# Kernel tuning notes

Measured on AMD Instinct MI355X. Metric: run time of the kernel, lower is better.

The kernel has to match this reference:

```python
import jax, jax.numpy as jnp
import numpy as np

DELTA = 1.5
EPS = 1e-7  # torch-em dice_score denominator clamp


def shift2d(t, off):
    # Equivalent to torch-em ReplicationPad + slice on the (already inverted)
    # offset: shifted[..., i, j] = t[..., clip(i + oy, 0, H-1), clip(j + ox, 0, W-1)]
    H, W = t.shape[-2], t.shape[-1]
    iy = jnp.clip(jnp.arange(H) + off[0], 0, H - 1)
    ix = jnp.clip(jnp.arange(W) + off[1], 0, W - 1)
    return t[..., iy, :][..., ix]


def dice_score_invert_sum(inp, tgt):
    # torch-em dice_score(invert=True, channelwise=True): channel axis = dim 1,
    # flatten everything else, sum of (1 - 2*num/den) over channels.
    num = jnp.einsum('bchw,bchw->c', inp, tgt)
    den = jnp.einsum('bchw,bchw->c', inp, inp) + jnp.einsum('bchw,bchw->c', tgt, tgt)
    score = 2.0 * num / jnp.maximum(den, EPS)
    return jnp.sum(1.0 - score)


def setup_inputs() -> dict:
    key = jax.random.key(0)
    k1, k2, k3 = jax.random.split(key, 3)
    B, E, H, W = 4, 12, 512, 512
    n_samples = 8
    input_ = jax.random.normal(k1, (B, E, H, W), dtype=jnp.float32)
    target = jax.random.randint(k2, (B, 1, H, W), 0, 50, dtype=jnp.int32)
    # offsets ~ randint(orange[0], orange[1]) per dim, i.e. values in [-27, -1]
    offsets = jax.random.randint(k3, (n_samples, 2), -27, 0, dtype=jnp.int32)
    return {"input_": input_, "target": target, "offsets": offsets}


def reference(input_, target, offsets):
    tgt = target.astype(jnp.float32)

    # embeddings -> affinities
    shifted_emb = jax.vmap(lambda o: shift2d(input_, o))(offsets)      # [S,B,E,H,W]
    ss = jnp.sum((input_[None] - shifted_emb) ** 2, axis=2)            # [S,B,H,W]
    norm = jnp.where(ss > 0, jnp.sqrt(jnp.where(ss > 0, ss, 1.0)), 0.0)
    affs = jnp.clip((2.0 * DELTA - norm) / (2.0 * DELTA), 0.0) ** 2
    affs = 1.0 - jnp.transpose(affs, (1, 0, 2, 3))                     # [B,S,H,W]

    # segmentation -> affinities
    shifted_seg = jax.vmap(lambda o: shift2d(tgt, o))(offsets)         # [S,B,1,H,W]
    target_affs = (tgt[None] == shifted_seg).astype(jnp.float32)[:, :, 0]
    target_affs = 1.0 - jnp.transpose(target_affs, (1, 0, 2, 3))       # [B,S,H,W]

    return dice_score_invert_sum(affs, target_affs)
```

## Files before the change

kernel.cpp:

```cpp
#include <hip/hip_runtime.h>


typedef float f2 __attribute__((ext_vector_type(2)));
typedef float f4 __attribute__((ext_vector_type(4)));

#define HWSZ   262144
#define NE     12
#define NC     13
#define NS     8
#define TROWS  16
#define TCOLS  64
#define NBLK   1024
#define HROWS  44
#define HCOLS  92
#define HSZ    (HROWS * HCOLS)
#define NCHUNK (HCOLS / 4)
#define NSLOT  (HSZ / 4)

__global__ __launch_bounds__(512) void affloss_main(
    const float* __restrict__ emb, const int* __restrict__ seg,
    const int* __restrict__ offs, float* __restrict__ partial) {
  __shared__ f4 buf4[NSLOT];
  __shared__ float red[8][16];
  float* buf = (float*)buf4;

  const int bid = blockIdx.x;
  const int nb  = (bid & 7) * (NBLK / 8) + (bid >> 3);
  const int b   = nb >> 8;
  const int rem = nb & 255;
  const int r0  = (rem >> 3) * TROWS;
  const int c0  = (rem & 7) * TCOLS;

  const int tid = threadIdx.x;
  const int tx  = tid & 31;
  const int row = tid >> 5;
  const int wv  = tid >> 6;

  const float* embB = emb + (size_t)b * NE * HWSZ;
  const int*   segB = seg + (size_t)b * HWSZ;

  int oyv[NS], oxv[NS];
  #pragma unroll
  for (int s = 0; s < NS; ++s) { oyv[s] = offs[2 * s]; oxv[s] = offs[2 * s + 1]; }

  int srow[2], sgc[2];
  #pragma unroll
  for (int k = 0; k < 2; ++k) {
    const int slot = tid + k * 512;
    const int rr = slot / NCHUNK;
    const int ch = slot - rr * NCHUNK;
    int gr = r0 - 28 + rr; gr = gr < 0 ? 0 : gr;
    srow[k] = gr;
    sgc[k] = c0 - 28 + 4 * ch;
  }
  const bool s1 = tid < (NSLOT - 512);

  auto stage_load = [&](int e, f4* r) {
    const float* p = (e < NE) ? (embB + (size_t)e * HWSZ) : (const float*)segB;
    #pragma unroll
    for (int k = 0; k < 2; ++k) {
      if (k == 1 && !s1) continue;
      const float* rowp = p + srow[k] * 512;
      if (sgc[k] >= 0) {
        r[k] = *reinterpret_cast<const f4*>(rowp + sgc[k]);
      } else {
        const float v = rowp[0];
        r[k] = f4{v, v, v, v};
      }
    }
  };
  auto stage_write = [&](const f4* r) {
    buf4[tid] = r[0];
    if (s1) buf4[tid + 512] = r[1];
  };

  f2 ssv[NS];
  #pragma unroll
  for (int s = 0; s < NS; ++s) ssv[s] = f2{0.f, 0.f};
  float numa[NS], dena[NS];
  #pragma unroll
  for (int s = 0; s < NS; ++s) { numa[s] = 0.f; dena[s] = 0.f; }

  const int cb = (row + 28) * HCOLS + 28 + 2 * tx;

  f4 r[2];
  stage_load(0, r);

  for (int e = 0; e < NC; ++e) {
    __syncthreads();
    stage_write(r);
    __syncthreads();
    if (e + 1 < NC) stage_load(e + 1, r);

    if (e < NE) {
      const f2 cc = *reinterpret_cast<const f2*>(&buf[cb]);
      #pragma unroll
      for (int s = 0; s < NS; ++s) {
        const int a = cb + oyv[s] * HCOLS + oxv[s];
        f2 sh; sh[0] = buf[a]; sh[1] = buf[a + 1];
        const f2 d = cc - sh;
        ssv[s][0] = fmaf(d[0], d[0], ssv[s][0]);
        ssv[s][1] = fmaf(d[1], d[1], ssv[s][1]);
      }
    } else {
      const int tc0 = __float_as_int(buf[cb]);
      const int tc1 = __float_as_int(buf[cb + 1]);
      #pragma unroll
      for (int s = 0; s < NS; ++s) {
        const int a = cb + oyv[s] * HCOLS + oxv[s];
        const int t0 = __float_as_int(buf[a]);
        const int t1 = __float_as_int(buf[a + 1]);
        {
          const float n  = __builtin_amdgcn_sqrtf(ssv[s][0]);
          const float rc = fmaxf(fmaf(n, -(1.0f / 3.0f), 1.0f), 0.0f);
          const float A  = fmaf(-rc, rc, 1.0f);
          const float ta = (tc0 == t0) ? 0.f : 1.f;
          numa[s] = fmaf(A, ta, numa[s]);
          dena[s] += fmaf(A, A, ta);
        }
        {
          const float n  = __builtin_amdgcn_sqrtf(ssv[s][1]);
          const float rc = fmaxf(fmaf(n, -(1.0f / 3.0f), 1.0f), 0.0f);
          const float A  = fmaf(-rc, rc, 1.0f);
          const float ta = (tc1 == t1) ? 0.f : 1.f;
          numa[s] = fmaf(A, ta, numa[s]);
          dena[s] += fmaf(A, A, ta);
        }
      }
    }
  }

  float arr[16];
  #pragma unroll
  for (int s = 0; s < NS; ++s) { arr[s] = numa[s]; arr[8 + s] = dena[s]; }
  #pragma unroll
  for (int k = 0; k < 16; ++k) {
    float v = arr[k];
    #pragma unroll
    for (int o = 32; o > 0; o >>= 1) v += __shfl_down(v, o, 64);
    arr[k] = v;
  }
  const int lane = tid & 63;
  if (lane == 0) {
    #pragma unroll
    for (int k = 0; k < 16; ++k) red[wv][k] = arr[k];
  }
  __syncthreads();
  if (tid < 16) {
    float v = 0.f;
    #pragma unroll
    for (int w = 0; w < 8; ++w) v += red[w][tid];
    partial[tid * NBLK + blockIdx.x] = v;
  }
}

__global__ __launch_bounds__(1024) void affloss_final(
    const float* __restrict__ partial, float* __restrict__ out) {
  __shared__ double csum[16];
  const int lane = threadIdx.x & 63, wv = threadIdx.x >> 6;

  double s = 0.0;
  for (int i = lane; i < NBLK; i += 64)
    s += (double)partial[wv * NBLK + i];
  #pragma unroll
  for (int o = 32; o > 0; o >>= 1) s += __shfl_down(s, o, 64);
  if (lane == 0) csum[wv] = s;
  __syncthreads();

  if (threadIdx.x == 0) {
    double total = 0.0;
    #pragma unroll
    for (int c = 0; c < 8; ++c) {
      double num = csum[c];
      double den = csum[8 + c];
      if (den < 1e-7) den = 1e-7;
      total += 1.0 - 2.0 * num / den;
    }
    out[0] = (float)total;
  }
}

extern "C" void kernel_launch(void* const* d_in, const int* in_sizes, int n_in,
                              void* d_out, int out_size, void* d_ws, size_t ws_size,
                              hipStream_t stream) {
  const float* emb  = (const float*)d_in[0];
  const int*   seg  = (const int*)d_in[1];
  const int*   offs = (const int*)d_in[2];
  float* partial = (float*)d_ws;

  affloss_main<<<NBLK, 512, 0, stream>>>(emb, seg, offs, partial);
  affloss_final<<<1, 1024, 0, stream>>>(partial, (float*)d_out);
}
```

Measured before the change: 43.66 us.

## Halve block size and give each thread four pixels strided by rows

Blocks drop from 512 to 256 threads. Each thread now owns four pixels in one column, spaced four rows apart, instead of two adjacent pixels. Each thread stages four f4 chunks of the halo tile per channel, and the shift offsets are precomputed as linear LDS offsets. The aim is more independent work and LDS loads per thread and fewer threads per block, trading higher register use for better latency hiding and occupancy balance.

Result: faster. 40.55 us, median of 2 (-7.1%).

```diff
diff --git a/kernel.cpp b/kernel.cpp
--- a/kernel.cpp
+++ b/kernel.cpp
@@ -1,7 +1,6 @@
 #include <hip/hip_runtime.h>
 
 
-typedef float f2 __attribute__((ext_vector_type(2)));
 typedef float f4 __attribute__((ext_vector_type(4)));
 
 #define HWSZ   262144
@@ -16,13 +15,14 @@
 #define HSZ    (HROWS * HCOLS)
 #define NCHUNK (HCOLS / 4)
 #define NSLOT  (HSZ / 4)
+#define QSTEP  (4 * HCOLS)
 
-__global__ __launch_bounds__(512) void affloss_main(
+__global__ __launch_bounds__(256) void affloss_main(
     const float* __restrict__ emb, const int* __restrict__ seg,
     const int* __restrict__ offs, float* __restrict__ partial) {
   __shared__ f4 buf4[NSLOT];
-  __shared__ float red[8][16];
-  float* buf = (float*)buf4;
+  __shared__ float red[4][16];
+  const float* buf = (const float*)buf4;
 
   const int bid = blockIdx.x;
   const int nb  = (bid & 7) * (NBLK / 8) + (bid >> 3);
@@ -31,35 +31,35 @@
   const int r0  = (rem >> 3) * TROWS;
   const int c0  = (rem & 7) * TCOLS;
 
-  const int tid = threadIdx.x;
-  const int tx  = tid & 31;
-  const int row = tid >> 5;
-  const int wv  = tid >> 6;
+  const int tid  = threadIdx.x;
+  const int lane = tid & 63;
+  const int w    = tid >> 6;
 
   const float* embB = emb + (size_t)b * NE * HWSZ;
   const int*   segB = seg + (size_t)b * HWSZ;
 
-  int oyv[NS], oxv[NS];
+  int soff[NS];
   #pragma unroll
-  for (int s = 0; s < NS; ++s) { oyv[s] = offs[2 * s]; oxv[s] = offs[2 * s + 1]; }
+  for (int s = 0; s < NS; ++s)
+    soff[s] = offs[2 * s] * HCOLS + offs[2 * s + 1];
 
-  int srow[2], sgc[2];
+  int srow[4], sgc[4];
   #pragma unroll
-  for (int k = 0; k < 2; ++k) {
-    const int slot = tid + k * 512;
+  for (int k = 0; k < 4; ++k) {
+    const int slot = tid + k * 256;
     const int rr = slot / NCHUNK;
     const int ch = slot - rr * NCHUNK;
     int gr = r0 - 28 + rr; gr = gr < 0 ? 0 : gr;
     srow[k] = gr;
     sgc[k] = c0 - 28 + 4 * ch;
   }
-  const bool s1 = tid < (NSLOT - 512);
+  const bool s3 = tid < (NSLOT - 3 * 256);
 
   auto stage_load = [&](int e, f4* r) {
     const float* p = (e < NE) ? (embB + (size_t)e * HWSZ) : (const float*)segB;
     #pragma unroll
-    for (int k = 0; k < 2; ++k) {
-      if (k == 1 && !s1) continue;
+    for (int k = 0; k < 4; ++k) {
+      if (k == 3 && !s3) continue;
       const float* rowp = p + srow[k] * 512;
       if (sgc[k] >= 0) {
         r[k] = *reinterpret_cast<const f4*>(rowp + sgc[k]);
@@ -70,20 +70,25 @@
     }
   };
   auto stage_write = [&](const f4* r) {
-    buf4[tid] = r[0];
-    if (s1) buf4[tid + 512] = r[1];
+    #pragma unroll
+    for (int k = 0; k < 4; ++k) {
+      if (k == 3 && !s3) continue;
+      buf4[tid + k * 256] = r[k];
+    }
   };
 
-  f2 ssv[NS];
+  float ssv[4][NS];
   #pragma unroll
-  for (int s = 0; s < NS; ++s) ssv[s] = f2{0.f, 0.f};
+  for (int q = 0; q < 4; ++q)
+    #pragma unroll
+    for (int s = 0; s < NS; ++s) ssv[q][s] = 0.f;
   float numa[NS], dena[NS];
   #pragma unroll
   for (int s = 0; s < NS; ++s) { numa[s] = 0.f; dena[s] = 0.f; }
 
-  const int cb = (row + 28) * HCOLS + 28 + 2 * tx;
+  const int cb0 = (28 + w) * HCOLS + 28 + lane;
 
-  f4 r[2];
+  f4 r[4];
   stage_load(0, r);
 
   for (int e = 0; e < NC; ++e) {
@@ -93,36 +98,33 @@
     if (e + 1 < NC) stage_load(e + 1, r);
 
     if (e < NE) {
-      const f2 cc = *reinterpret_cast<const f2*>(&buf[cb]);
+      float cc[4];
+      #pragma unroll
+      for (int q = 0; q < 4; ++q) cc[q] = buf[cb0 + QSTEP * q];
       #pragma unroll
       for (int s = 0; s < NS; ++s) {
-        const int a = cb + oyv[s] * HCOLS + oxv[s];
-        f2 sh; sh[0] = buf[a]; sh[1] = buf[a + 1];
-        const f2 d = cc - sh;
-        ssv[s][0] = fmaf(d[0], d[0], ssv[s][0]);
-        ssv[s][1] = fmaf(d[1], d[1], ssv[s][1]);
+        const int a = cb0 + soff[s];
+        #pragma unroll
+        for (int q = 0; q < 4; ++q) {
+          const float sh = buf[a + QSTEP * q];
+          const float d = cc[q] - sh;
+          ssv[q][s] = fmaf(d, d, ssv[q][s]);
+        }
       }
     } else {
-      const int tc0 = __float_as_int(buf[cb]);
-      const int tc1 = __float_as_int(buf[cb + 1]);
+      int tc[4];
+      #pragma unroll
+      for (int q = 0; q < 4; ++q) tc[q] = __float_as_int(buf[cb0 + QSTEP * q]);
       #pragma unroll
       for (int s = 0; s < NS; ++s) {
-        const int a = cb + oyv[s] * HCOLS + oxv[s];
-        const int t0 = __float_as_int(buf[a]);
-        const int t1 = __float_as_int(buf[a + 1]);
-        {
-          const float n  = __builtin_amdgcn_sqrtf(ssv[s][0]);
+        const int a = cb0 + soff[s];
+        #pragma unroll
+        for (int q = 0; q < 4; ++q) {
+          const int t = __float_as_int(buf[a + QSTEP * q]);
+          const float n  = __builtin_amdgcn_sqrtf(ssv[q][s]);
           const float rc = fmaxf(fmaf(n, -(1.0f / 3.0f), 1.0f), 0.0f);
           const float A  = fmaf(-rc, rc, 1.0f);
-          const float ta = (tc0 == t0) ? 0.f : 1.f;
-          numa[s] = fmaf(A, ta, numa[s]);
-          dena[s] += fmaf(A, A, ta);
-        }
-        {
-          const float n  = __builtin_amdgcn_sqrtf(ssv[s][1]);
-          const float rc = fmaxf(fmaf(n, -(1.0f / 3.0f), 1.0f), 0.0f);
-          const float A  = fmaf(-rc, rc, 1.0f);
-          const float ta = (tc1 == t1) ? 0.f : 1.f;
+          const float ta = (tc[q] == t) ? 0.f : 1.f;
           numa[s] = fmaf(A, ta, numa[s]);
           dena[s] += fmaf(A, A, ta);
         }
@@ -140,16 +142,13 @@
     for (int o = 32; o > 0; o >>= 1) v += __shfl_down(v, o, 64);
     arr[k] = v;
   }
-  const int lane = tid & 63;
   if (lane == 0) {
     #pragma unroll
-    for (int k = 0; k < 16; ++k) red[wv][k] = arr[k];
+    for (int k = 0; k < 16; ++k) red[w][k] = arr[k];
   }
   __syncthreads();
   if (tid < 16) {
-    float v = 0.f;
-    #pragma unroll
-    for (int w = 0; w < 8; ++w) v += red[w][tid];
+    float v = red[0][tid] + red[1][tid] + red[2][tid] + red[3][tid];
     partial[tid * NBLK + blockIdx.x] = v;
   }
 }
@@ -188,6 +187,6 @@
   const int*   offs = (const int*)d_in[2];
   float* partial = (float*)d_ws;
 
-  affloss_main<<<NBLK, 512, 0, stream>>>(emb, seg, offs, partial);
+  affloss_main<<<NBLK, 256, 0, stream>>>(emb, seg, offs, partial);
   affloss_final<<<1, 1024, 0, stream>>>(partial, (float*)d_out);
 }
```
